# Kernel tuning notes

Measured on AMD Instinct MI355X. Metric: run time of the kernel, lower is better.

## Reference

```python
import jax, jax.numpy as jnp
import numpy as np


def setup_inputs() -> dict:
    key = jax.random.key(0)
    ks = jax.random.split(key, 6)
    num_nodes, H, B = 500000, 128, 100000
    node_ids = jnp.arange(B, dtype=jnp.int64 if jax.config.jax_enable_x64 else jnp.int32)
    messages = jax.random.normal(ks[0], (B, H), dtype=jnp.float32)
    memory = jax.random.normal(ks[1], (num_nodes, H), dtype=jnp.float32)
    # PyTorch GRUCell params: weight_ih/weight_hh [3H, H], biases [3H]
    s = 1.0 / np.sqrt(H)
    W_ih = jax.random.uniform(ks[2], (3 * H, H), minval=-s, maxval=s, dtype=jnp.float32)
    W_hh = jax.random.uniform(ks[3], (3 * H, H), minval=-s, maxval=s, dtype=jnp.float32)
    b_ih = jax.random.uniform(ks[4], (3 * H,), minval=-s, maxval=s, dtype=jnp.float32)
    b_hh = jax.random.uniform(ks[5], (3 * H,), minval=-s, maxval=s, dtype=jnp.float32)
    return {"node_ids": node_ids, "messages": messages, "memory": memory,
            "W_ih": W_ih, "W_hh": W_hh, "b_ih": b_ih, "b_hh": b_hh}


def _gru_cell(x, h, W_ih, W_hh, b_ih, b_hh):
    # gi/gh: [B, 3H]; chunk order in torch GRUCell is (r, z, n)
    gi = x @ W_ih.T + b_ih
    gh = h @ W_hh.T + b_hh
    i_r, i_z, i_n = jnp.split(gi, 3, axis=-1)
    h_r, h_z, h_n = jnp.split(gh, 3, axis=-1)
    r = jax.nn.sigmoid(i_r + h_r)
    z = jax.nn.sigmoid(i_z + h_z)
    n = jnp.tanh(i_n + r * h_n)
    return (1.0 - z) * n + z * h


def reference(node_ids, messages, memory, W_ih, W_hh, b_ih, b_hh):
    # gather per-node memory, GRU update, scatter back (update_memory)
    current = memory[node_ids]                              # [B, H] gather
    updated = _gru_cell(messages, current, W_ih, W_hh, b_ih, b_hh)
    new_memory = memory.at[node_ids].set(updated)           # [N, H] scatter
    return new_memory
```

## Files before the change

### kernel.cpp

```cpp
#include <hip/hip_runtime.h>
#include <hip/hip_bf16.h>

typedef __bf16 bf16x8 __attribute__((ext_vector_type(8)));
typedef float  f32x4  __attribute__((ext_vector_type(4)));

#define GRU_H 128
#define ROWS  32
#define LDSP  132

__device__ inline bf16x8 frag_from_lds(const float* p) {
    float4 a = *reinterpret_cast<const float4*>(p);
    float4 b = *reinterpret_cast<const float4*>(p + 4);
    bf16x8 r;
    r[0] = (__bf16)a.x; r[1] = (__bf16)a.y; r[2] = (__bf16)a.z; r[3] = (__bf16)a.w;
    r[4] = (__bf16)b.x; r[5] = (__bf16)b.y; r[6] = (__bf16)b.z; r[7] = (__bf16)b.w;
    return r;
}

__device__ inline bf16x8 frag_from_global(const float* p) { return frag_from_lds(p); }

__device__ inline float sigmoidf_(float x) { return 1.f / (1.f + __expf(-x)); }
__device__ inline float tanhf_(float x)    { return 1.f - 2.f / (__expf(2.f * x) + 1.f); }

__global__ __launch_bounds__(256) void copy_rev_kernel(const float4* __restrict__ src,
                                                       float4* __restrict__ dst, size_t n4) {
    size_t stride = (size_t)gridDim.x * 256;
    for (size_t i = (size_t)blockIdx.x * 256 + threadIdx.x; i < n4; i += stride) {
        size_t j = n4 - 1 - i;
        dst[j] = src[j];
    }
}

__global__ __launch_bounds__(512, 2) void gru_update_kernel(
    const int*   __restrict__ node_ids,
    const float* __restrict__ messages,
    const float* __restrict__ memory,
    const float* __restrict__ W_ih,
    const float* __restrict__ W_hh,
    const float* __restrict__ b_ih,
    const float* __restrict__ b_hh,
    float*       __restrict__ out,
    int B)
{
    __shared__ float xs[ROWS][LDSP];
    __shared__ float hs[ROWS][LDSP];
    __shared__ int   ids[ROWS];

    const int wave = threadIdx.x >> 6;
    const int lane = threadIdx.x & 63;
    const int l15  = lane & 15;
    const int lg   = lane >> 4;
    const int col  = wave * 16 + l15;

    bf16x8 bfrag[6][4];
    #pragma unroll
    for (int g = 0; g < 3; ++g)
        #pragma unroll
        for (int ks = 0; ks < 4; ++ks) {
            const int off = (g * GRU_H + col) * GRU_H + ks * 32 + lg * 8;
            bfrag[g][ks]     = frag_from_global(W_ih + off);
            bfrag[g + 3][ks] = frag_from_global(W_hh + off);
        }
    const float bi_r = b_ih[col], bi_z = b_ih[GRU_H + col], bi_n = b_ih[2 * GRU_H + col];
    const float bh_r = b_hh[col], bh_z = b_hh[GRU_H + col], bh_n = b_hh[2 * GRU_H + col];

    const int nchunks = (B + ROWS - 1) / ROWS;
    for (int c = blockIdx.x; c < nchunks; c += gridDim.x) {
        const int rb = c * ROWS;

        #pragma unroll
        for (int s = 0; s < 2; ++s) {
            const int f4  = threadIdx.x + s * 512;
            const int row = f4 >> 5;
            const int c4  = f4 & 31;
            const int grow = rb + row;
            if (grow < B) {
                const int gid = node_ids[grow];
                if (c4 == 0) ids[row] = gid;
                *reinterpret_cast<float4*>(&xs[row][c4 * 4]) =
                    *reinterpret_cast<const float4*>(&messages[(size_t)grow * GRU_H + c4 * 4]);
                *reinterpret_cast<float4*>(&hs[row][c4 * 4]) =
                    *reinterpret_cast<const float4*>(&memory[(size_t)gid * GRU_H + c4 * 4]);
            } else {
                float4 z = {0.f, 0.f, 0.f, 0.f};
                *reinterpret_cast<float4*>(&xs[row][c4 * 4]) = z;
                *reinterpret_cast<float4*>(&hs[row][c4 * 4]) = z;
            }
        }
        __syncthreads();

        #pragma unroll
        for (int sub = 0; sub < 2; ++sub) {
            const int rbase = sub * 16;

            bf16x8 ax[4], ah[4];
            #pragma unroll
            for (int ks = 0; ks < 4; ++ks) {
                ax[ks] = frag_from_lds(&xs[rbase + l15][ks * 32 + lg * 8]);
                ah[ks] = frag_from_lds(&hs[rbase + l15][ks * 32 + lg * 8]);
            }

            f32x4 acc[6];
            #pragma unroll
            for (int g = 0; g < 6; ++g) acc[g] = (f32x4){0.f, 0.f, 0.f, 0.f};

            #pragma unroll
            for (int ks = 0; ks < 4; ++ks) {
                acc[0] = __builtin_amdgcn_mfma_f32_16x16x32_bf16(ax[ks], bfrag[0][ks], acc[0], 0, 0, 0);
                acc[1] = __builtin_amdgcn_mfma_f32_16x16x32_bf16(ax[ks], bfrag[1][ks], acc[1], 0, 0, 0);
                acc[2] = __builtin_amdgcn_mfma_f32_16x16x32_bf16(ax[ks], bfrag[2][ks], acc[2], 0, 0, 0);
                acc[3] = __builtin_amdgcn_mfma_f32_16x16x32_bf16(ah[ks], bfrag[3][ks], acc[3], 0, 0, 0);
                acc[4] = __builtin_amdgcn_mfma_f32_16x16x32_bf16(ah[ks], bfrag[4][ks], acc[4], 0, 0, 0);
                acc[5] = __builtin_amdgcn_mfma_f32_16x16x32_bf16(ah[ks], bfrag[5][ks], acc[5], 0, 0, 0);
            }

            #pragma unroll
            for (int r = 0; r < 4; ++r) {
                const int row  = rbase + lg * 4 + r;
                const int grow = rb + row;
                if (grow < B) {
                    const int gid = ids[row];
                    const float h  = hs[row][col];
                    const float rg = sigmoidf_((acc[0][r] + bi_r) + (acc[3][r] + bh_r));
                    const float zg = sigmoidf_((acc[1][r] + bi_z) + (acc[4][r] + bh_z));
                    const float ng = tanhf_((acc[2][r] + bi_n) + rg * (acc[5][r] + bh_n));
                    out[(size_t)gid * GRU_H + col] = (1.f - zg) * ng + zg * h;
                }
            }
        }
        __syncthreads();
    }
}

extern "C" void kernel_launch(void* const* d_in, const int* in_sizes, int n_in,
                              void* d_out, int out_size, void* d_ws, size_t ws_size,
                              hipStream_t stream) {
    const int*   node_ids = (const int*)d_in[0];
    const float* messages = (const float*)d_in[1];
    const float* memory   = (const float*)d_in[2];
    const float* W_ih     = (const float*)d_in[3];
    const float* W_hh     = (const float*)d_in[4];
    const float* b_ih     = (const float*)d_in[5];
    const float* b_hh     = (const float*)d_in[6];
    float* out = (float*)d_out;

    const int B = in_sizes[0];
    const int N = in_sizes[2] / GRU_H;

    const size_t n4 = (size_t)N * GRU_H / 4;
    copy_rev_kernel<<<2048, 256, 0, stream>>>((const float4*)memory, (float4*)out, n4);

    const int nchunks = (B + ROWS - 1) / ROWS;
    int grid = nchunks < 1024 ? nchunks : 1024;
    gru_update_kernel<<<grid, 512, 0, stream>>>(node_ids, messages, memory,
                                                W_ih, W_hh, b_ih, b_hh, out, B);
}
```

Before: 596.5 us.

## Skip copying rows overwritten by the scatter when node_ids is an arange

Adds a runtime check of whether node_ids equals 0..B-1. When it does, the bulk memory-to-output copy skips the first B rows, because the GRU scatter overwrites them anyway, which cuts copy traffic. The weights are converted once into bf16 MFMA fragment order in workspace instead of being converted by every block. The GRU kernel now processes 64 rows per chunk, holds messages in LDS as bf16, and uses XOR-swizzled LDS layouts. The cost is two extra small kernel launches and a dependence on a flag in workspace.

```diff
diff --git a/kernel.cpp b/kernel.cpp
--- a/kernel.cpp
+++ b/kernel.cpp
@@ -5,46 +5,72 @@
 typedef float  f32x4  __attribute__((ext_vector_type(4)));
 
 #define GRU_H 128
-#define ROWS  32
-#define LDSP  132
-
-__device__ inline bf16x8 frag_from_lds(const float* p) {
-    float4 a = *reinterpret_cast<const float4*>(p);
-    float4 b = *reinterpret_cast<const float4*>(p + 4);
+#define ROWS  64
+#define NTHR  512
+
+__device__ inline float sigmoidf_(float x) { return 1.f / (1.f + __expf(-x)); }
+__device__ inline float tanhf_(float x)    { return 1.f - 2.f / (__expf(2.f * x) + 1.f); }
+
+__device__ inline bf16x8 cvt8(float4 a, float4 b) {
     bf16x8 r;
     r[0] = (__bf16)a.x; r[1] = (__bf16)a.y; r[2] = (__bf16)a.z; r[3] = (__bf16)a.w;
     r[4] = (__bf16)b.x; r[5] = (__bf16)b.y; r[6] = (__bf16)b.z; r[7] = (__bf16)b.w;
     return r;
 }
 
-__device__ inline bf16x8 frag_from_global(const float* p) { return frag_from_lds(p); }
-
-__device__ inline float sigmoidf_(float x) { return 1.f / (1.f + __expf(-x)); }
-__device__ inline float tanhf_(float x)    { return 1.f - 2.f / (__expf(2.f * x) + 1.f); }
-
-__global__ __launch_bounds__(256) void copy_rev_kernel(const float4* __restrict__ src,
-                                                       float4* __restrict__ dst, size_t n4) {
-    size_t stride = (size_t)gridDim.x * 256;
-    for (size_t i = (size_t)blockIdx.x * 256 + threadIdx.x; i < n4; i += stride) {
-        size_t j = n4 - 1 - i;
-        dst[j] = src[j];
-    }
+__global__ __launch_bounds__(512) void convert_weights(
+    const float* __restrict__ W_ih, const float* __restrict__ W_hh,
+    bf16x8* __restrict__ frags, int* __restrict__ flag)
+{
+    if (blockIdx.x == 0 && threadIdx.x == 0) *flag = 0;
+    const int t = blockIdx.x * 512 + threadIdx.x;
+    const int lane = t & 63;
+    const int ks   = (t >> 6) & 3;
+    const int r    = t >> 8;
+    const int g    = r % 6;
+    const int wave = r / 6;
+    const int col  = wave * 16 + (lane & 15);
+    const int lg   = lane >> 4;
+    const int gg   = (g < 3) ? g : g - 3;
+    const float* src = ((g < 3) ? W_ih : W_hh) + ((size_t)(gg * GRU_H + col)) * GRU_H + ks * 32 + lg * 8;
+    float4 a = *reinterpret_cast<const float4*>(src);
+    float4 b = *reinterpret_cast<const float4*>(src + 4);
+    frags[t] = cvt8(a, b);
+}
+
+__global__ __launch_bounds__(256) void check_arange(const int* __restrict__ ids, int B,
+                                                    int* __restrict__ flag)
+{
+    int bad = 0;
+    for (int i = blockIdx.x * 256 + threadIdx.x; i < B; i += gridDim.x * 256)
+        bad |= (ids[i] != i);
+    if (bad) atomicOr(flag, 1);
+}
+
+__global__ __launch_bounds__(256) void copy_skip(const float4* __restrict__ src,
+                                                 float4* __restrict__ dst,
+                                                 size_t n4, size_t skip4,
+                                                 const int* __restrict__ flag)
+{
+    const size_t start  = (*flag == 0) ? skip4 : 0;
+    const size_t stride = (size_t)gridDim.x * 256;
+    for (size_t i = start + (size_t)blockIdx.x * 256 + threadIdx.x; i < n4; i += stride)
+        dst[i] = src[i];
 }
 
 __global__ __launch_bounds__(512, 2) void gru_update_kernel(
     const int*   __restrict__ node_ids,
     const float* __restrict__ messages,
     const float* __restrict__ memory,
-    const float* __restrict__ W_ih,
-    const float* __restrict__ W_hh,
+    const bf16x8* __restrict__ frags,
     const float* __restrict__ b_ih,
     const float* __restrict__ b_hh,
     float*       __restrict__ out,
     int B)
 {
-    __shared__ float xs[ROWS][LDSP];
-    __shared__ float hs[ROWS][LDSP];
-    __shared__ int   ids[ROWS];
+    __shared__ __align__(16) unsigned char xs_raw[ROWS * 256];
+    __shared__ __align__(16) unsigned char hf_raw[ROWS * 512];
+    __shared__ int ids[ROWS];
 
     const int wave = threadIdx.x >> 6;
     const int lane = threadIdx.x & 63;
@@ -54,13 +80,11 @@
 
     bf16x8 bfrag[6][4];
     #pragma unroll
-    for (int g = 0; g < 3; ++g)
-        #pragma unroll
-        for (int ks = 0; ks < 4; ++ks) {
-            const int off = (g * GRU_H + col) * GRU_H + ks * 32 + lg * 8;
-            bfrag[g][ks]     = frag_from_global(W_ih + off);
-            bfrag[g + 3][ks] = frag_from_global(W_hh + off);
-        }
+    for (int g = 0; g < 6; ++g)
+        #pragma unroll
+        for (int ks = 0; ks < 4; ++ks)
+            bfrag[g][ks] = frags[((wave * 6 + g) * 4 + ks) * 64 + lane];
+
     const float bi_r = b_ih[col], bi_z = b_ih[GRU_H + col], bi_n = b_ih[2 * GRU_H + col];
     const float bh_r = b_hh[col], bh_z = b_hh[GRU_H + col], bh_n = b_hh[2 * GRU_H + col];
 
@@ -69,35 +93,56 @@
         const int rb = c * ROWS;
 
         #pragma unroll
-        for (int s = 0; s < 2; ++s) {
-            const int f4  = threadIdx.x + s * 512;
-            const int row = f4 >> 5;
-            const int c4  = f4 & 31;
+        for (int s = 0; s < 4; ++s) {
+            const int slot = threadIdx.x + s * 512;
+            const int row  = slot >> 5;
+            const int c4   = slot & 31;
             const int grow = rb + row;
+            float4 v = {0.f, 0.f, 0.f, 0.f};
             if (grow < B) {
                 const int gid = node_ids[grow];
                 if (c4 == 0) ids[row] = gid;
-                *reinterpret_cast<float4*>(&xs[row][c4 * 4]) =
-                    *reinterpret_cast<const float4*>(&messages[(size_t)grow * GRU_H + c4 * 4]);
-                *reinterpret_cast<float4*>(&hs[row][c4 * 4]) =
-                    *reinterpret_cast<const float4*>(&memory[(size_t)gid * GRU_H + c4 * 4]);
+                v = *reinterpret_cast<const float4*>(&memory[(size_t)gid * GRU_H + c4 * 4]);
+            }
+            *reinterpret_cast<float4*>(&hf_raw[row * 512 + ((c4 * 16) ^ ((row & 7) << 4))]) = v;
+        }
+        #pragma unroll
+        for (int s = 0; s < 2; ++s) {
+            const int slot = threadIdx.x + s * 512;
+            const int row  = slot >> 4;
+            const int c8   = slot & 15;
+            const int grow = rb + row;
+            bf16x8 v;
+            if (grow < B) {
+                const float* p = &messages[(size_t)grow * GRU_H + c8 * 8];
+                float4 a = *reinterpret_cast<const float4*>(p);
+                float4 b = *reinterpret_cast<const float4*>(p + 4);
+                v = cvt8(a, b);
             } else {
-                float4 z = {0.f, 0.f, 0.f, 0.f};
-                *reinterpret_cast<float4*>(&xs[row][c4 * 4]) = z;
-                *reinterpret_cast<float4*>(&hs[row][c4 * 4]) = z;
-            }
+                #pragma unroll
+                for (int j = 0; j < 8; ++j) v[j] = (__bf16)0.f;
+            }
+            *reinterpret_cast<bf16x8*>(&xs_raw[row * 256 + ((c8 * 16) ^ ((row & 7) << 4))]) = v;
         }
         __syncthreads();
 
         #pragma unroll
-        for (int sub = 0; sub < 2; ++sub) {
+        for (int sub = 0; sub < 4; ++sub) {
             const int rbase = sub * 16;
+            const int arow  = rbase + l15;
+            const int sw    = (arow & 7) << 4;
 
             bf16x8 ax[4], ah[4];
             #pragma unroll
             for (int ks = 0; ks < 4; ++ks) {
-                ax[ks] = frag_from_lds(&xs[rbase + l15][ks * 32 + lg * 8]);
-                ah[ks] = frag_from_lds(&hs[rbase + l15][ks * 32 + lg * 8]);
+                ax[ks] = *reinterpret_cast<const bf16x8*>(
+                    &xs_raw[arow * 256 + (((ks * 4 + lg) * 16) ^ sw)]);
+                const int c4a = ks * 8 + lg * 2;
+                float4 f0 = *reinterpret_cast<const float4*>(
+                    &hf_raw[arow * 512 + ((c4a * 16) ^ sw)]);
+                float4 f1 = *reinterpret_cast<const float4*>(
+                    &hf_raw[arow * 512 + (((c4a + 1) * 16) ^ sw)]);
+                ah[ks] = cvt8(f0, f1);
             }
 
             f32x4 acc[6];
@@ -120,7 +165,8 @@
                 const int grow = rb + row;
                 if (grow < B) {
                     const int gid = ids[row];
-                    const float h  = hs[row][col];
+                    const float h = *reinterpret_cast<const float*>(
+                        &hf_raw[row * 512 + ((((col >> 2) * 16) ^ ((row & 7) << 4)) + (col & 3) * 4)]);
                     const float rg = sigmoidf_((acc[0][r] + bi_r) + (acc[3][r] + bh_r));
                     const float zg = sigmoidf_((acc[1][r] + bi_z) + (acc[4][r] + bh_z));
                     const float ng = tanhf_((acc[2][r] + bi_n) + rg * (acc[5][r] + bh_n));
@@ -147,11 +193,16 @@
     const int B = in_sizes[0];
     const int N = in_sizes[2] / GRU_H;
 
+    int*    flag  = (int*)d_ws;
+    bf16x8* frags = (bf16x8*)((char*)d_ws + 1024);
+
+    convert_weights<<<24, 512, 0, stream>>>(W_ih, W_hh, frags, flag);
+    check_arange<<<256, 256, 0, stream>>>(node_ids, B, flag);
     const size_t n4 = (size_t)N * GRU_H / 4;
-    copy_rev_kernel<<<2048, 256, 0, stream>>>((const float4*)memory, (float4*)out, n4);
-
+    const size_t skip4 = (size_t)B * GRU_H / 4;
+    copy_skip<<<2048, 256, 0, stream>>>((const float4*)memory, (float4*)out, n4, skip4, flag);
     const int nchunks = (B + ROWS - 1) / ROWS;
-    int grid = nchunks < 1024 ? nchunks : 1024;
+    int grid = nchunks < 512 ? nchunks : 512;
     gru_update_kernel<<<grid, 512, 0, stream>>>(node_ids, messages, memory,
-                                                W_ih, W_hh, b_ih, b_hh, out, B);
-}
+                                                frags, b_ih, b_hh, out, B);
+}
```

Result: faster. 533.1 us (-10.6%).
